# Kernel tuning notes

Hardware: AMD Instinct MI355X
Metric: run time of the kernel (lower is better)

Reference implementation:

```python
import jax, jax.numpy as jnp
import numpy as np

TOP_P = 0.95        # sample() default topp
TEMPERATURE = 0.8   # token_temperature
NEG_INF = float('-inf')


def setup_inputs() -> dict:
    key = jax.random.key(0)
    k1, k2 = jax.random.split(key)
    B, V = 8192, 2048  # batch rows x speech-unit vocab
    logits = jax.random.normal(k1, (B, V), dtype=jnp.float32) * 4.0
    # uniform noise for Gumbel-max multinomial sampling (open interval)
    u = jax.random.uniform(k2, (B, V), dtype=jnp.float32, minval=1e-6, maxval=1.0 - 1e-6)
    return {"logits": logits, "u": u}


def _top_p_filter(logits, p):
    # descending sort (matches torch.sort(descending=True))
    order = jnp.argsort(-logits, axis=-1)                      # [B, V]
    sorted_logits = jnp.take_along_axis(logits, order, axis=-1)
    cum = jnp.cumsum(jax.nn.softmax(sorted_logits, axis=-1), axis=-1)
    remove = cum > p
    # shift right by one so the first token above the threshold is kept
    remove = jnp.concatenate(
        [jnp.zeros_like(remove[..., :1]), remove[..., :-1]], axis=-1)
    # scatter mask back to unsorted order via inverse permutation
    inv = jnp.argsort(order, axis=-1)
    remove_unsorted = jnp.take_along_axis(remove, inv, axis=-1)
    return jnp.where(remove_unsorted, NEG_INF, logits)


def reference(logits, u):
    scaled = logits / TEMPERATURE
    filtered = _top_p_filter(scaled, TOP_P)                    # [B, V]
    probs = jax.nn.softmax(filtered, axis=-1)                  # [B, V]
    # multinomial(probs, 1) == Gumbel-max over filtered logits
    gumbel = -jnp.log(-jnp.log(u))
    sampled = jnp.argmax(filtered + gumbel, axis=-1, keepdims=True)  # [B, 1]
    return sampled, probs
```

## Files before the change

### kernel.cpp

```cpp
#include <hip/hip_runtime.h>
#include <math.h>

#define VOCAB 2048
#define TPB   256
#define NBINS 64
#define BIN_SCALE 6.0f
#define BCAP  512
#define KCAP  512

typedef float vf4 __attribute__((ext_vector_type(4)));

__device__ __forceinline__ unsigned long long pack_key(float z, int idx) {
    unsigned zb = __float_as_uint(z);
    zb = (zb & 0x80000000u) ? ~zb : (zb | 0x80000000u);
    return ((unsigned long long)zb << 32) | (unsigned)(VOCAB - 1 - idx);
}

__global__ __launch_bounds__(TPB, 8) void sampler_kernel(
    const float* __restrict__ logits,
    const float* __restrict__ uni,
    float* __restrict__ out_idx,
    float* __restrict__ out_probs)
{
    const int row  = blockIdx.x;
    const int t    = threadIdx.x;
    const int lane = t & 63;
    const int wid  = t >> 6;

    __shared__ float  s_bins[NBINS];
    __shared__ float  s_wf[4];
    __shared__ double s_wd[4];
    __shared__ unsigned long long s_key[4];
    __shared__ int    s_cnt, s_cnt2;
    __shared__ float  s_cv[BCAP];
    __shared__ float  s_ce[BCAP];
    __shared__ float  s_kv[KCAP];
    __shared__ float  s_ku[KCAP];
    __shared__ int    s_ki[KCAP];

    const float* lrow = logits    + (size_t)row * VOCAB;
    const float* urow = uni       + (size_t)row * VOCAB;
    float*       prow = out_probs + (size_t)row * VOCAB;

    if (t < NBINS) s_bins[t] = 0.0f;
    if (t == 0) { s_cnt = 0; s_cnt2 = 0; }

    const vf4 a0 = *(const vf4*)(lrow + 4 * t);
    const vf4 a1 = *(const vf4*)(lrow + VOCAB / 2 + 4 * t);
    const vf4 u0 = *(const vf4*)(urow + 4 * t);
    const vf4 u1 = *(const vf4*)(urow + VOCAB / 2 + 4 * t);
    float s[8]  = {a0.x * 1.25f, a0.y * 1.25f, a0.z * 1.25f, a0.w * 1.25f,
                   a1.x * 1.25f, a1.y * 1.25f, a1.z * 1.25f, a1.w * 1.25f};
    float uu[8] = {u0.x, u0.y, u0.z, u0.w, u1.x, u1.y, u1.z, u1.w};

    float lm = s[0];
    #pragma unroll
    for (int j = 1; j < 8; j++) lm = fmaxf(lm, s[j]);
    #pragma unroll
    for (int off = 32; off; off >>= 1) lm = fmaxf(lm, __shfl_down(lm, off));
    if (lane == 0) s_wf[wid] = lm;
    __syncthreads();
    const float m = fmaxf(fmaxf(s_wf[0], s_wf[1]), fmaxf(s_wf[2], s_wf[3]));

    float e[8];
    float psum = 0.0f;
    #pragma unroll
    for (int j = 0; j < 8; j++) {
        e[j] = __expf(s[j] - m);
        psum += e[j];
        int b = (int)((m - s[j]) * BIN_SCALE);
        if (b < NBINS) atomicAdd(&s_bins[b], e[j]);
    }
    double dp = (double)psum;
    #pragma unroll
    for (int off = 32; off; off >>= 1) dp += __shfl_down(dp, off);
    if (lane == 0) s_wd[wid] = dp;
    __syncthreads();

    const double S  = s_wd[0] + s_wd[1] + s_wd[2] + s_wd[3];
    const double pS = 0.95 * S;
    const float  bf = s_bins[lane];
    double c = (double)bf;
    #pragma unroll
    for (int d = 1; d < 64; d <<= 1) {
        double o = __shfl_up(c, d);
        if (lane >= d) c += o;
    }
    unsigned long long ball = __ballot(c > pS);
    const int    bstar     = ball ? (__ffsll(ball) - 1) : (NBINS - 1);
    const double cumBefore = __shfl(c - (double)bf, bstar);

    #pragma unroll
    for (int j = 0; j < 8; j++) {
        int b = (int)((m - s[j]) * BIN_SCALE);
        if (b == bstar) {
            int pos = atomicAdd(&s_cnt, 1);
            if (pos < BCAP) { s_cv[pos] = s[j]; s_ce[pos] = e[j]; }
        }
    }
    __syncthreads();
    const int cnt = min(s_cnt, BCAP);

    float SKb = 0.0f;
    for (int i = 0; i < cnt; i++) {
        float vi = s_cv[i], part = 0.0f;
        for (int jj = 0; jj < cnt; jj++)
            part += (s_cv[jj] > vi) ? s_ce[jj] : 0.0f;
        if (cumBefore + (double)part <= pS) SKb += s_ce[i];
    }
    const float invSK = 1.0f / (float)(cumBefore + (double)SKb);

    unsigned keptMask = 0;
    #pragma unroll
    for (int j = 0; j < 8; j++) {
        int  b = (int)((m - s[j]) * BIN_SCALE);
        bool kept;
        if (b < bstar)      kept = true;
        else if (b > bstar) kept = false;
        else {
            float part = 0.0f;
            for (int i = 0; i < cnt; i++)
                part += (s_cv[i] > s[j]) ? s_ce[i] : 0.0f;
            kept = (cumBefore + (double)part) <= pS;
        }
        if (kept) keptMask |= (1u << j);
    }

    vf4 p0, p1;
    p0.x = (keptMask & 0x01) ? e[0] * invSK : 0.0f;
    p0.y = (keptMask & 0x02) ? e[1] * invSK : 0.0f;
    p0.z = (keptMask & 0x04) ? e[2] * invSK : 0.0f;
    p0.w = (keptMask & 0x08) ? e[3] * invSK : 0.0f;
    p1.x = (keptMask & 0x10) ? e[4] * invSK : 0.0f;
    p1.y = (keptMask & 0x20) ? e[5] * invSK : 0.0f;
    p1.z = (keptMask & 0x40) ? e[6] * invSK : 0.0f;
    p1.w = (keptMask & 0x80) ? e[7] * invSK : 0.0f;
    __builtin_nontemporal_store(p0, (vf4*)(prow + 4 * t));
    __builtin_nontemporal_store(p1, (vf4*)(prow + VOCAB / 2 + 4 * t));

    unsigned long long ovKey = 0ull;
    #pragma unroll
    for (int j = 0; j < 8; j++) {
        if ((keptMask >> j) & 1u) {
            int idx = (j < 4) ? (4 * t + j) : (VOCAB / 2 + 4 * t + (j - 4));
            int pos = atomicAdd(&s_cnt2, 1);
            if (pos < KCAP) { s_kv[pos] = s[j]; s_ku[pos] = uu[j]; s_ki[pos] = idx; }
            else {
                float z = s[j] + (-logf(-logf(uu[j])));
                unsigned long long kk = pack_key(z, idx);
                ovKey = (kk > ovKey) ? kk : ovKey;
            }
        }
    }
    __syncthreads();
    const int k  = s_cnt2;
    const int kl = min(k, KCAP);

    unsigned long long key = ovKey;
    for (int i = t; i < kl; i += TPB) {
        float z = s_kv[i] + (-logf(-logf(s_ku[i])));
        unsigned long long kk = pack_key(z, s_ki[i]);
        key = (kk > key) ? kk : key;
    }

    if (k <= 64) {
        if (wid == 0) {
            #pragma unroll
            for (int off = 32; off; off >>= 1) {
                unsigned long long ok = __shfl_down(key, off);
                key = (ok > key) ? ok : key;
            }
            if (lane == 0)
                out_idx[row] = (float)(VOCAB - 1 - (int)(key & 0xFFFFFFFFu));
        }
    } else {
        #pragma unroll
        for (int off = 32; off; off >>= 1) {
            unsigned long long ok = __shfl_down(key, off);
            key = (ok > key) ? ok : key;
        }
        if (lane == 0) s_key[wid] = key;
        __syncthreads();
        if (t == 0) {
            unsigned long long k0 = s_key[0];
            #pragma unroll
            for (int w = 1; w < 4; w++) k0 = (s_key[w] > k0) ? s_key[w] : k0;
            out_idx[row] = (float)(VOCAB - 1 - (int)(k0 & 0xFFFFFFFFu));
        }
    }
}

extern "C" void kernel_launch(void* const* d_in, const int* in_sizes, int n_in,
                              void* d_out, int out_size, void* d_ws, size_t ws_size,
                              hipStream_t stream) {
    const float* logits = (const float*)d_in[0];
    const float* u      = (const float*)d_in[1];
    const int B = in_sizes[0] / VOCAB;
    float* out_idx   = (float*)d_out;
    float* out_probs = (float*)d_out + B;
    sampler_kernel<<<B, TPB, 0, stream>>>(logits, u, out_idx, out_probs);
}
```

Measured before the change: 184.2 us.

## Load noise only for kept tokens and reduce Gumbel keys directly per thread

Instead of loading the full uniform-noise row up front, each thread now reads u only for tokens that survive the top-p filter, using scalar gathered loads. The shared-memory compaction of kept tokens (values, noise, indices, counter) is replaced by a per-thread max followed by a wave and block reduction. Bin indices are cached in registers rather than recomputed. This cuts global read traffic on u and shared-memory use, which may raise occupancy, at the cost of uncoalesced scalar loads issued late in the kernel and log work spread unevenly across threads.

After: 183.8 us. Within noise of the previous version (-0.2%).

```diff
diff --git a/kernel.cpp b/kernel.cpp
--- a/kernel.cpp
+++ b/kernel.cpp
@@ -6,7 +6,6 @@
 #define NBINS 64
 #define BIN_SCALE 6.0f
 #define BCAP  512
-#define KCAP  512
 
 typedef float vf4 __attribute__((ext_vector_type(4)));
 
@@ -31,27 +30,21 @@
     __shared__ float  s_wf[4];
     __shared__ double s_wd[4];
     __shared__ unsigned long long s_key[4];
-    __shared__ int    s_cnt, s_cnt2;
+    __shared__ int    s_cnt;
     __shared__ float  s_cv[BCAP];
     __shared__ float  s_ce[BCAP];
-    __shared__ float  s_kv[KCAP];
-    __shared__ float  s_ku[KCAP];
-    __shared__ int    s_ki[KCAP];
 
     const float* lrow = logits    + (size_t)row * VOCAB;
     const float* urow = uni       + (size_t)row * VOCAB;
     float*       prow = out_probs + (size_t)row * VOCAB;
 
     if (t < NBINS) s_bins[t] = 0.0f;
-    if (t == 0) { s_cnt = 0; s_cnt2 = 0; }
+    if (t == 0) s_cnt = 0;
 
     const vf4 a0 = *(const vf4*)(lrow + 4 * t);
     const vf4 a1 = *(const vf4*)(lrow + VOCAB / 2 + 4 * t);
-    const vf4 u0 = *(const vf4*)(urow + 4 * t);
-    const vf4 u1 = *(const vf4*)(urow + VOCAB / 2 + 4 * t);
-    float s[8]  = {a0.x * 1.25f, a0.y * 1.25f, a0.z * 1.25f, a0.w * 1.25f,
-                   a1.x * 1.25f, a1.y * 1.25f, a1.z * 1.25f, a1.w * 1.25f};
-    float uu[8] = {u0.x, u0.y, u0.z, u0.w, u1.x, u1.y, u1.z, u1.w};
+    float s[8] = {a0.x * 1.25f, a0.y * 1.25f, a0.z * 1.25f, a0.w * 1.25f,
+                  a1.x * 1.25f, a1.y * 1.25f, a1.z * 1.25f, a1.w * 1.25f};
 
     float lm = s[0];
     #pragma unroll
@@ -63,13 +56,14 @@
     const float m = fmaxf(fmaxf(s_wf[0], s_wf[1]), fmaxf(s_wf[2], s_wf[3]));
 
     float e[8];
+    int   bin[8];
     float psum = 0.0f;
     #pragma unroll
     for (int j = 0; j < 8; j++) {
         e[j] = __expf(s[j] - m);
         psum += e[j];
-        int b = (int)((m - s[j]) * BIN_SCALE);
-        if (b < NBINS) atomicAdd(&s_bins[b], e[j]);
+        bin[j] = (int)((m - s[j]) * BIN_SCALE);
+        if (bin[j] < NBINS) atomicAdd(&s_bins[bin[j]], e[j]);
     }
     double dp = (double)psum;
     #pragma unroll
@@ -92,8 +86,7 @@
 
     #pragma unroll
     for (int j = 0; j < 8; j++) {
-        int b = (int)((m - s[j]) * BIN_SCALE);
-        if (b == bstar) {
+        if (bin[j] == bstar) {
             int pos = atomicAdd(&s_cnt, 1);
             if (pos < BCAP) { s_cv[pos] = s[j]; s_ce[pos] = e[j]; }
         }
@@ -113,10 +106,9 @@
     unsigned keptMask = 0;
     #pragma unroll
     for (int j = 0; j < 8; j++) {
-        int  b = (int)((m - s[j]) * BIN_SCALE);
         bool kept;
-        if (b < bstar)      kept = true;
-        else if (b > bstar) kept = false;
+        if (bin[j] < bstar)      kept = true;
+        else if (bin[j] > bstar) kept = false;
         else {
             float part = 0.0f;
             for (int i = 0; i < cnt; i++)
@@ -138,55 +130,29 @@
     __builtin_nontemporal_store(p0, (vf4*)(prow + 4 * t));
     __builtin_nontemporal_store(p1, (vf4*)(prow + VOCAB / 2 + 4 * t));
 
-    unsigned long long ovKey = 0ull;
+    unsigned long long key = 0ull;
     #pragma unroll
     for (int j = 0; j < 8; j++) {
         if ((keptMask >> j) & 1u) {
-            int idx = (j < 4) ? (4 * t + j) : (VOCAB / 2 + 4 * t + (j - 4));
-            int pos = atomicAdd(&s_cnt2, 1);
-            if (pos < KCAP) { s_kv[pos] = s[j]; s_ku[pos] = uu[j]; s_ki[pos] = idx; }
-            else {
-                float z = s[j] + (-logf(-logf(uu[j])));
-                unsigned long long kk = pack_key(z, idx);
-                ovKey = (kk > ovKey) ? kk : ovKey;
-            }
+            int   idx = (j < 4) ? (4 * t + j) : (VOCAB / 2 + 4 * t + (j - 4));
+            float uv  = urow[idx];
+            float z   = s[j] + (-logf(-logf(uv)));
+            unsigned long long kk = pack_key(z, idx);
+            key = (kk > key) ? kk : key;
         }
     }
+    #pragma unroll
+    for (int off = 32; off; off >>= 1) {
+        unsigned long long ok = __shfl_down(key, off);
+        key = (ok > key) ? ok : key;
+    }
+    if (lane == 0) s_key[wid] = key;
     __syncthreads();
-    const int k  = s_cnt2;
-    const int kl = min(k, KCAP);
-
-    unsigned long long key = ovKey;
-    for (int i = t; i < kl; i += TPB) {
-        float z = s_kv[i] + (-logf(-logf(s_ku[i])));
-        unsigned long long kk = pack_key(z, s_ki[i]);
-        key = (kk > key) ? kk : key;
-    }
-
-    if (k <= 64) {
-        if (wid == 0) {
-            #pragma unroll
-            for (int off = 32; off; off >>= 1) {
-                unsigned long long ok = __shfl_down(key, off);
-                key = (ok > key) ? ok : key;
-            }
-            if (lane == 0)
-                out_idx[row] = (float)(VOCAB - 1 - (int)(key & 0xFFFFFFFFu));
-        }
-    } else {
+    if (t == 0) {
+        unsigned long long k0 = s_key[0];
         #pragma unroll
-        for (int off = 32; off; off >>= 1) {
-            unsigned long long ok = __shfl_down(key, off);
-            key = (ok > key) ? ok : key;
-        }
-        if (lane == 0) s_key[wid] = key;
-        __syncthreads();
-        if (t == 0) {
-            unsigned long long k0 = s_key[0];
-            #pragma unroll
-            for (int w = 1; w < 4; w++) k0 = (s_key[w] > k0) ? s_key[w] : k0;
-            out_idx[row] = (float)(VOCAB - 1 - (int)(k0 & 0xFFFFFFFFu));
-        }
+        for (int w = 1; w < 4; w++) k0 = (s_key[w] > k0) ? s_key[w] : k0;
+        out_idx[row] = (float)(VOCAB - 1 - (int)(k0 & 0xFFFFFFFFu));
     }
 }
 
```

## Process four rows per block, prefetch next logits, gather noise only for kept tokens

Applied to the files above, without the earlier changes.

Each block now loops over four rows and prefetches the next row's logits while the current row is processed. The dense read of the uniform-noise row is replaced by indexed global reads for only the tokens that survive top-p, which cuts read traffic. Exponentials are recomputed instead of kept in registers, and the shared buffer caps are halved to lower register and LDS pressure. In exchange, block count drops fourfold, the noise gathers are scattered and uncoalesced, and rows within a block are processed serially.

After: 185.3 us. About the same (+0.6%).

```diff
diff --git a/kernel.cpp b/kernel.cpp
--- a/kernel.cpp
+++ b/kernel.cpp
@@ -3,10 +3,10 @@
 
 #define VOCAB 2048
 #define TPB   256
+#define ROWS  4
 #define NBINS 64
 #define BIN_SCALE 6.0f
-#define BCAP  512
-#define KCAP  512
+#define BCAP  256
 
 typedef float vf4 __attribute__((ext_vector_type(4)));
 
@@ -22,171 +22,182 @@
     float* __restrict__ out_idx,
     float* __restrict__ out_probs)
 {
-    const int row  = blockIdx.x;
     const int t    = threadIdx.x;
     const int lane = t & 63;
     const int wid  = t >> 6;
-
-    __shared__ float  s_bins[NBINS];
+    const int row0 = blockIdx.x * ROWS;
+
+    __shared__ float  s_bins[ROWS][NBINS];
     __shared__ float  s_wf[4];
     __shared__ double s_wd[4];
     __shared__ unsigned long long s_key[4];
-    __shared__ int    s_cnt, s_cnt2;
+    __shared__ int    s_cnt[ROWS], s_cnt2[ROWS];
     __shared__ float  s_cv[BCAP];
     __shared__ float  s_ce[BCAP];
-    __shared__ float  s_kv[KCAP];
-    __shared__ float  s_ku[KCAP];
-    __shared__ int    s_ki[KCAP];
-
-    const float* lrow = logits    + (size_t)row * VOCAB;
-    const float* urow = uni       + (size_t)row * VOCAB;
-    float*       prow = out_probs + (size_t)row * VOCAB;
-
-    if (t < NBINS) s_bins[t] = 0.0f;
-    if (t == 0) { s_cnt = 0; s_cnt2 = 0; }
-
-    const vf4 a0 = *(const vf4*)(lrow + 4 * t);
-    const vf4 a1 = *(const vf4*)(lrow + VOCAB / 2 + 4 * t);
-    const vf4 u0 = *(const vf4*)(urow + 4 * t);
-    const vf4 u1 = *(const vf4*)(urow + VOCAB / 2 + 4 * t);
-    float s[8]  = {a0.x * 1.25f, a0.y * 1.25f, a0.z * 1.25f, a0.w * 1.25f,
-                   a1.x * 1.25f, a1.y * 1.25f, a1.z * 1.25f, a1.w * 1.25f};
-    float uu[8] = {u0.x, u0.y, u0.z, u0.w, u1.x, u1.y, u1.z, u1.w};
-
-    float lm = s[0];
+    __shared__ float  s_kv[BCAP];
+    __shared__ int    s_ki[BCAP];
+
+    ((float*)s_bins)[t] = 0.0f;
+    if (t < ROWS) { s_cnt[t] = 0; s_cnt2[t] = 0; }
+
+    vf4 c0 = *(const vf4*)(logits + (size_t)row0 * VOCAB + t * 4);
+    vf4 c1 = *(const vf4*)(logits + (size_t)row0 * VOCAB + VOCAB / 2 + t * 4);
+
     #pragma unroll
-    for (int j = 1; j < 8; j++) lm = fmaxf(lm, s[j]);
-    #pragma unroll
-    for (int off = 32; off; off >>= 1) lm = fmaxf(lm, __shfl_down(lm, off));
-    if (lane == 0) s_wf[wid] = lm;
-    __syncthreads();
-    const float m = fmaxf(fmaxf(s_wf[0], s_wf[1]), fmaxf(s_wf[2], s_wf[3]));
-
-    float e[8];
-    float psum = 0.0f;
-    #pragma unroll
-    for (int j = 0; j < 8; j++) {
-        e[j] = __expf(s[j] - m);
-        psum += e[j];
-        int b = (int)((m - s[j]) * BIN_SCALE);
-        if (b < NBINS) atomicAdd(&s_bins[b], e[j]);
-    }
-    double dp = (double)psum;
-    #pragma unroll
-    for (int off = 32; off; off >>= 1) dp += __shfl_down(dp, off);
-    if (lane == 0) s_wd[wid] = dp;
-    __syncthreads();
-
-    const double S  = s_wd[0] + s_wd[1] + s_wd[2] + s_wd[3];
-    const double pS = 0.95 * S;
-    const float  bf = s_bins[lane];
-    double c = (double)bf;
-    #pragma unroll
-    for (int d = 1; d < 64; d <<= 1) {
-        double o = __shfl_up(c, d);
-        if (lane >= d) c += o;
-    }
-    unsigned long long ball = __ballot(c > pS);
-    const int    bstar     = ball ? (__ffsll(ball) - 1) : (NBINS - 1);
-    const double cumBefore = __shfl(c - (double)bf, bstar);
-
-    #pragma unroll
-    for (int j = 0; j < 8; j++) {
-        int b = (int)((m - s[j]) * BIN_SCALE);
-        if (b == bstar) {
-            int pos = atomicAdd(&s_cnt, 1);
-            if (pos < BCAP) { s_cv[pos] = s[j]; s_ce[pos] = e[j]; }
-        }
-    }
-    __syncthreads();
-    const int cnt = min(s_cnt, BCAP);
-
-    float SKb = 0.0f;
-    for (int i = 0; i < cnt; i++) {
-        float vi = s_cv[i], part = 0.0f;
-        for (int jj = 0; jj < cnt; jj++)
-            part += (s_cv[jj] > vi) ? s_ce[jj] : 0.0f;
-        if (cumBefore + (double)part <= pS) SKb += s_ce[i];
-    }
-    const float invSK = 1.0f / (float)(cumBefore + (double)SKb);
-
-    unsigned keptMask = 0;
-    #pragma unroll
-    for (int j = 0; j < 8; j++) {
-        int  b = (int)((m - s[j]) * BIN_SCALE);
-        bool kept;
-        if (b < bstar)      kept = true;
-        else if (b > bstar) kept = false;
-        else {
-            float part = 0.0f;
-            for (int i = 0; i < cnt; i++)
-                part += (s_cv[i] > s[j]) ? s_ce[i] : 0.0f;
-            kept = (cumBefore + (double)part) <= pS;
-        }
-        if (kept) keptMask |= (1u << j);
-    }
-
-    vf4 p0, p1;
-    p0.x = (keptMask & 0x01) ? e[0] * invSK : 0.0f;
-    p0.y = (keptMask & 0x02) ? e[1] * invSK : 0.0f;
-    p0.z = (keptMask & 0x04) ? e[2] * invSK : 0.0f;
-    p0.w = (keptMask & 0x08) ? e[3] * invSK : 0.0f;
-    p1.x = (keptMask & 0x10) ? e[4] * invSK : 0.0f;
-    p1.y = (keptMask & 0x20) ? e[5] * invSK : 0.0f;
-    p1.z = (keptMask & 0x40) ? e[6] * invSK : 0.0f;
-    p1.w = (keptMask & 0x80) ? e[7] * invSK : 0.0f;
-    __builtin_nontemporal_store(p0, (vf4*)(prow + 4 * t));
-    __builtin_nontemporal_store(p1, (vf4*)(prow + VOCAB / 2 + 4 * t));
-
-    unsigned long long ovKey = 0ull;
-    #pragma unroll
-    for (int j = 0; j < 8; j++) {
-        if ((keptMask >> j) & 1u) {
-            int idx = (j < 4) ? (4 * t + j) : (VOCAB / 2 + 4 * t + (j - 4));
-            int pos = atomicAdd(&s_cnt2, 1);
-            if (pos < KCAP) { s_kv[pos] = s[j]; s_ku[pos] = uu[j]; s_ki[pos] = idx; }
+    for (int r = 0; r < ROWS; r++) {
+        const int    row  = row0 + r;
+        const float* urow = uni       + (size_t)row * VOCAB;
+        float*       prow = out_probs + (size_t)row * VOCAB;
+
+        vf4 n0, n1;
+        if (r + 1 < ROWS) {
+            n0 = *(const vf4*)(logits + (size_t)(row + 1) * VOCAB + t * 4);
+            n1 = *(const vf4*)(logits + (size_t)(row + 1) * VOCAB + VOCAB / 2 + t * 4);
+        }
+
+        float s[8] = {c0.x * 1.25f, c0.y * 1.25f, c0.z * 1.25f, c0.w * 1.25f,
+                      c1.x * 1.25f, c1.y * 1.25f, c1.z * 1.25f, c1.w * 1.25f};
+
+        float lm = s[0];
+        #pragma unroll
+        for (int j = 1; j < 8; j++) lm = fmaxf(lm, s[j]);
+        #pragma unroll
+        for (int off = 32; off; off >>= 1) lm = fmaxf(lm, __shfl_xor(lm, off));
+        if (lane == 0) s_wf[wid] = lm;
+        __syncthreads();
+        const float m = fmaxf(fmaxf(s_wf[0], s_wf[1]), fmaxf(s_wf[2], s_wf[3]));
+
+        float psum = 0.0f;
+        #pragma unroll
+        for (int j = 0; j < 8; j++) {
+            float e = __expf(s[j] - m);
+            psum += e;
+            int b = (int)((m - s[j]) * BIN_SCALE);
+            if (b < NBINS) atomicAdd(&s_bins[r][b], e);
+        }
+        double dp = (double)psum;
+        #pragma unroll
+        for (int off = 32; off; off >>= 1) dp += __shfl_xor(dp, off);
+        if (lane == 0) s_wd[wid] = dp;
+        __syncthreads();
+
+        const double S  = s_wd[0] + s_wd[1] + s_wd[2] + s_wd[3];
+        const double pS = 0.95 * S;
+        const float  bf = s_bins[r][lane];
+        double c = (double)bf;
+        #pragma unroll
+        for (int d = 1; d < 64; d <<= 1) {
+            double o = __shfl_up(c, d);
+            if (lane >= d) c += o;
+        }
+        unsigned long long ball = __ballot(c > pS);
+        const int    bstar     = ball ? (__ffsll(ball) - 1) : (NBINS - 1);
+        const double cumBefore = __shfl(c - (double)bf, bstar);
+
+        #pragma unroll
+        for (int j = 0; j < 8; j++) {
+            int b = (int)((m - s[j]) * BIN_SCALE);
+            if (b == bstar) {
+                int pos = atomicAdd(&s_cnt[r], 1);
+                if (pos < BCAP) { s_cv[pos] = s[j]; s_ce[pos] = __expf(s[j] - m); }
+            }
+        }
+        __syncthreads();
+        const int cnt = min(s_cnt[r], BCAP);
+
+        float SKb = 0.0f;
+        for (int i = 0; i < cnt; i++) {
+            float vi = s_cv[i], part = 0.0f;
+            for (int jj = 0; jj < cnt; jj++)
+                part += (s_cv[jj] > vi) ? s_ce[jj] : 0.0f;
+            if (cumBefore + (double)part <= pS) SKb += s_ce[i];
+        }
+        const float invSK = 1.0f / (float)(cumBefore + (double)SKb);
+
+        unsigned keptMask = 0;
+        #pragma unroll
+        for (int j = 0; j < 8; j++) {
+            int  b = (int)((m - s[j]) * BIN_SCALE);
+            bool kept;
+            if (b < bstar)      kept = true;
+            else if (b > bstar) kept = false;
             else {
-                float z = s[j] + (-logf(-logf(uu[j])));
-                unsigned long long kk = pack_key(z, idx);
-                ovKey = (kk > ovKey) ? kk : ovKey;
-            }
-        }
-    }
-    __syncthreads();
-    const int k  = s_cnt2;
-    const int kl = min(k, KCAP);
-
-    unsigned long long key = ovKey;
-    for (int i = t; i < kl; i += TPB) {
-        float z = s_kv[i] + (-logf(-logf(s_ku[i])));
-        unsigned long long kk = pack_key(z, s_ki[i]);
-        key = (kk > key) ? kk : key;
-    }
-
-    if (k <= 64) {
-        if (wid == 0) {
+                float part = 0.0f;
+                for (int i = 0; i < cnt; i++)
+                    part += (s_cv[i] > s[j]) ? s_ce[i] : 0.0f;
+                kept = (cumBefore + (double)part) <= pS;
+            }
+            if (kept) keptMask |= (1u << j);
+        }
+
+        vf4 p0, p1;
+        p0.x = (keptMask & 0x01) ? __expf(s[0] - m) * invSK : 0.0f;
+        p0.y = (keptMask & 0x02) ? __expf(s[1] - m) * invSK : 0.0f;
+        p0.z = (keptMask & 0x04) ? __expf(s[2] - m) * invSK : 0.0f;
+        p0.w = (keptMask & 0x08) ? __expf(s[3] - m) * invSK : 0.0f;
+        p1.x = (keptMask & 0x10) ? __expf(s[4] - m) * invSK : 0.0f;
+        p1.y = (keptMask & 0x20) ? __expf(s[5] - m) * invSK : 0.0f;
+        p1.z = (keptMask & 0x40) ? __expf(s[6] - m) * invSK : 0.0f;
+        p1.w = (keptMask & 0x80) ? __expf(s[7] - m) * invSK : 0.0f;
+        __builtin_nontemporal_store(p0, (vf4*)(prow + t * 4));
+        __builtin_nontemporal_store(p1, (vf4*)(prow + VOCAB / 2 + t * 4));
+
+        unsigned long long ovKey = 0ull;
+        #pragma unroll
+        for (int j = 0; j < 8; j++) {
+            if ((keptMask >> j) & 1u) {
+                int idx = (j < 4) ? (t * 4 + j) : (VOCAB / 2 + t * 4 + (j - 4));
+                int pos = atomicAdd(&s_cnt2[r], 1);
+                if (pos < BCAP) { s_kv[pos] = s[j]; s_ki[pos] = idx; }
+                else {
+                    float z = s[j] + (-logf(-logf(urow[idx])));
+                    unsigned long long kk = pack_key(z, idx);
+                    ovKey = (kk > ovKey) ? kk : ovKey;
+                }
+            }
+        }
+        __syncthreads();
+        const int k = s_cnt2[r];
+
+        if (k <= BCAP) {
+            if (wid == 0) {
+                unsigned long long key = 0ull;
+                for (int i = lane; i < k; i += 64) {
+                    float z = s_kv[i] + (-logf(-logf(urow[s_ki[i]])));
+                    unsigned long long kk = pack_key(z, s_ki[i]);
+                    key = (kk > key) ? kk : key;
+                }
+                #pragma unroll
+                for (int off = 32; off; off >>= 1) {
+                    unsigned long long ok = __shfl_xor(key, off);
+                    key = (ok > key) ? ok : key;
+                }
+                if (lane == 0)
+                    out_idx[row] = (float)(VOCAB - 1 - (int)(key & 0xFFFFFFFFu));
+            }
+        } else {
+            unsigned long long key = ovKey;
+            for (int i = t; i < BCAP; i += TPB) {
+                float z = s_kv[i] + (-logf(-logf(urow[s_ki[i]])));
+                unsigned long long kk = pack_key(z, s_ki[i]);
+                key = (kk > key) ? kk : key;
+            }
             #pragma unroll
             for (int off = 32; off; off >>= 1) {
-                unsigned long long ok = __shfl_down(key, off);
+                unsigned long long ok = __shfl_xor(key, off);
                 key = (ok > key) ? ok : key;
             }
-            if (lane == 0)
-                out_idx[row] = (float)(VOCAB - 1 - (int)(key & 0xFFFFFFFFu));
-        }
-    } else {
-        #pragma unroll
-        for (int off = 32; off; off >>= 1) {
-            unsigned long long ok = __shfl_down(key, off);
-            key = (ok > key) ? ok : key;
-        }
-        if (lane == 0) s_key[wid] = key;
-        __syncthreads();
-        if (t == 0) {
-            unsigned long long k0 = s_key[0];
-            #pragma unroll
-            for (int w = 1; w < 4; w++) k0 = (s_key[w] > k0) ? s_key[w] : k0;
-            out_idx[row] = (float)(VOCAB - 1 - (int)(k0 & 0xFFFFFFFFu));
-        }
+            if (lane == 0) s_key[wid] = key;
+            __syncthreads();
+            if (t == 0) {
+                unsigned long long k0 = s_key[0];
+                #pragma unroll
+                for (int w = 1; w < 4; w++) k0 = (s_key[w] > k0) ? s_key[w] : k0;
+                out_idx[row] = (float)(VOCAB - 1 - (int)(k0 & 0xFFFFFFFFu));
+            }
+        }
+
+        c0 = n0; c1 = n1;
     }
 }
 
@@ -198,5 +209,5 @@
     const int B = in_sizes[0] / VOCAB;
     float* out_idx   = (float*)d_out;
     float* out_probs = (float*)d_out + B;
-    sampler_kernel<<<B, TPB, 0, stream>>>(logits, u, out_idx, out_probs);
+    sampler_kernel<<<B / ROWS, TPB, 0, stream>>>(logits, u, out_idx, out_probs);
 }
```
